# Optimization experiments

Hardware: AMD Instinct MI355X
Metric: run time of the kernel (lower is better)

Reference implementation:

```python
import jax, jax.numpy as jnp
import numpy as np

N = 8          # num_nodes (forced: stack with deconv output of leading dim 64 = 8*8)
T = 10         # out_dim == num_steps (Conv1d(out_dim, 1, ...) runs over the time axis)
H = 64         # hidden_dim (forced: ConvTranspose1d in_channels=64)
E = 2 * N      # edges come in fwd/rev pairs; E/2 must equal N for avg_pool squeeze
NODE_IN = 512  # gat1 in_dim = x_feat width (510) + CNN_1 output (2)
EDGE_IN = 128


def _conv1d(x, w, b, pad):
    # x: [B, Cin, L], w: [Cout, Cin, K]
    y = jax.lax.conv_general_dilated(x, w, (1,), [(pad, pad)],
                                     dimension_numbers=('NCH', 'OIH', 'NCH'))
    return y + b[None, :, None]


def _gat(x, src, dst, ea, W, a_s, a_d, We, a_e, bias, heads, ch, concat):
    # PyG GATConv with edge_dim and default add_self_loops=True (mean-fill edge_attr)
    n = x.shape[0]
    loop = jnp.arange(n)
    src = jnp.concatenate([src, loop])
    dst = jnp.concatenate([dst, loop])
    ea = jnp.concatenate([ea, jnp.broadcast_to(ea.mean(0), (n, ea.shape[1]))], 0)
    h = (x @ W).reshape(n, heads, ch)                 # [N,H,C]
    he = (ea @ We).reshape(-1, heads, ch)             # [E+N,H,C]
    alpha = (h * a_s).sum(-1)[src] + (h * a_d).sum(-1)[dst] + (he * a_e).sum(-1)
    alpha = jax.nn.leaky_relu(alpha, 0.2)             # [E+N,H]
    amax = jax.ops.segment_max(alpha, dst, num_segments=n)
    ex = jnp.exp(alpha - amax[dst])
    den = jax.ops.segment_sum(ex, dst, num_segments=n)
    w = ex / (den[dst] + 1e-16)                       # scatter-softmax over dst
    out = jax.ops.segment_sum(w[:, :, None] * h[src], dst, num_segments=n)
    out = out.reshape(n, heads * ch) if concat else out.mean(1)
    return out + bias


def _forward(x_feat, x_feat_tmp, edge_attr, c1w1, c1b1, c1w2, c1b2,
             g1_lin, g1_as, g1_ad, g1_le, g1_ae, g1_b,
             g2_lin, g2_as, g2_ad, g2_le, g2_ae, g2_b,
             mlp_w1, mlp_b1, mlp_w2, mlp_b2,
             d1w, d1b, d2w, d2b, d3w, d3b,
             c2w1, c2b1, c2w2, c2b2, c2l1w, c2l1b, c2l2w, c2l2b,
             edge_index):
    src, dst = edge_index[0], edge_index[1]
    # ---- CNN_1 on rows 1 and 5 of x_feat_tmp ----
    t = jnp.stack([x_feat_tmp[1], x_feat_tmp[5]], axis=1)    # [N,2,T]
    t = t.reshape(2, N, T)                                   # torch .view semantics
    t = jax.nn.relu(_conv1d(t, c1w1, c1b1, 1))               # [2,N,T]
    t = _conv1d(jnp.transpose(t, (0, 2, 1)), c1w2, c1b2, 1)  # [2,1,N]
    x_ = jax.nn.relu(t.reshape(N, 2))                        # torch .view semantics
    # ---- GAT stack ----
    x = jnp.concatenate([x_feat, x_], axis=1)                # [N,512]
    x = jax.nn.relu(_gat(x, src, dst, edge_attr, g1_lin, g1_as, g1_ad,
                         g1_le, g1_ae, g1_b, 4, H, True))    # [N,256]
    ea_new = jax.nn.relu(edge_attr @ mlp_w1 + mlp_b1) @ mlp_w2 + mlp_b2  # [E,64]
    x = jax.nn.relu(_gat(x, src, dst, ea_new, g2_lin, g2_as, g2_ad,
                         g2_le, g2_ae, g2_b, 1, H, False))   # [N,64]
    # ---- ConvTranspose1d on length-1 input == einsum; avg_pool2d over nodes/edges ----
    x_pool = (jnp.einsum('ni,iot->not', x, d1w) + d1b[None, :, None]).mean(0)          # [64,10]
    ef = (jnp.einsum('ni,iot->not', ea_new[::2], d2w) + d2b[None, :, None]).mean(0)    # [64,10]
    er = (jnp.einsum('ni,iot->not', ea_new[1::2], d3w) + d3b[None, :, None]).mean(0)   # [64,10]
    inf = x_feat_tmp.reshape(N * N, T)                       # [64,10]
    # ---- CNN_2 ----
    c = jnp.stack([x_pool, inf, ef, er], axis=1)             # [64,4,10]
    c = _conv1d(c, c2w1, c2b1, 0)                            # [64,32,8]
    c = c.reshape(N * N, 32, 4, 2).max(-1)                   # MaxPool1d(2) -> [64,32,4]
    c = _conv1d(c, c2w2, c2b2, 0)                            # [64,64,2]
    c = c.reshape(N * N, 128)                                # Flatten(1,2)
    c = jax.nn.relu((c @ c2l1w + c2l1b) @ c2l2w + c2l2b)     # [64,10]
    return c.reshape(N, N, T)


def setup_inputs():
    ks = iter(jax.random.split(jax.random.key(0), 48))
    def rn(shape, s=0.1):
        return jax.random.normal(next(ks), shape, dtype=jnp.float32) * s
    return dict(
        x_feat=rn((N, NODE_IN - 2), 1.0),
        x_feat_tmp=rn((N, N, T), 1.0),
        edge_attr=rn((E, EDGE_IN), 1.0),
        c1w1=rn((N, N, 3)), c1b1=rn((N,)),
        c1w2=rn((1, T, 3)), c1b2=rn((1,)),
        g1_lin=rn((NODE_IN, 4 * H)), g1_as=rn((4, H)), g1_ad=rn((4, H)),
        g1_le=rn((EDGE_IN, 4 * H)), g1_ae=rn((4, H)), g1_b=rn((4 * H,)),
        g2_lin=rn((4 * H, H)), g2_as=rn((1, H)), g2_ad=rn((1, H)),
        g2_le=rn((H, H)), g2_ae=rn((1, H)), g2_b=rn((H,)),
        mlp_w1=rn((EDGE_IN, H)), mlp_b1=rn((H,)),
        mlp_w2=rn((H, H)), mlp_b2=rn((H,)),
        d1w=rn((H, H, 10)), d1b=rn((H,)),
        d2w=rn((H, H, 10)), d2b=rn((H,)),
        d3w=rn((H, H, 10)), d3b=rn((H,)),
        c2w1=rn((32, 4, 3)), c2b1=rn((32,)),
        c2w2=rn((64, 32, 3)), c2b2=rn((64,)),
        c2l1w=rn((128, 256)), c2l1b=rn((256,)),
        c2l2w=rn((256, T)), c2l2b=rn((T,)),
        edge_index=jax.random.randint(next(ks), (2, E), 0, N, dtype=jnp.int32),
    )


def reference(x_feat, x_feat_tmp, edge_attr, c1w1, c1b1, c1w2, c1b2,
              g1_lin, g1_as, g1_ad, g1_le, g1_ae, g1_b,
              g2_lin, g2_as, g2_ad, g2_le, g2_ae, g2_b,
              mlp_w1, mlp_b1, mlp_w2, mlp_b2,
              d1w, d1b, d2w, d2b, d3w, d3b,
              c2w1, c2b1, c2w2, c2b2, c2l1w, c2l1b, c2l2w, c2l2b,
              edge_index):
    return _forward(x_feat, x_feat_tmp, edge_attr, c1w1, c1b1, c1w2, c1b2,
                    g1_lin, g1_as, g1_ad, g1_le, g1_ae, g1_b,
                    g2_lin, g2_as, g2_ad, g2_le, g2_ae, g2_b,
                    mlp_w1, mlp_b1, mlp_w2, mlp_b2,
                    d1w, d1b, d2w, d2b, d3w, d3b,
                    c2w1, c2b1, c2w2, c2b2, c2l1w, c2l1b, c2l2w, c2l2b,
                    edge_index)
```

## Files before the change

### kernel.cpp

```cpp
#include <hip/hip_runtime.h>
#include <math.h>

#define WS_HXPART 0
#define WS_SMALL  8192
#define SM_XCNN 0
#define SM_SE1A 16
#define SM_SE1B 84
#define SM_SE2  152
#define SM_WF   172
#define SM_BF   1452
#define SM_VME  1462
#define SM_SIZE 1600

#define F_H    0
#define F_X1   2048
#define F_H2P  4096
#define F_GL0  6144
#define F_GL1  6400
#define F_G1AS 6656
#define F_G1AD 6912
#define F_G1B  7168
#define F_SS1  7424
#define F_SD1  7456
#define F_MX1  7488
#define F_DN1  7520
#define F_WT1  7552
#define F_SW2  7680
#define F_A1   7680
#define F_H2   7936
#define F_X2   8448
#define F_G2AS 8960
#define F_G2AD 9024
#define F_G2B  9088
#define F_SS2  9152
#define F_SD2  9160
#define F_MX2  9168
#define F_DN2  9176
#define F_A2   9184
#define F_WT2  9248
#define F_SML  13824
#define F_SW1  15424
#define F_CIN  15808
#define F_ESRC 15968
#define F_EDST 15992
#define F_SB1  16016
#define F_SB2  16048
#define F_SDB  16112
#define F_VM0  16128
#define SM_TOT 16192

__global__ __launch_bounds__(256) void k1_pre(
    const float* __restrict__ xf,   const float* __restrict__ xft,
    const float* __restrict__ ea,
    const float* __restrict__ c1w1, const float* __restrict__ c1b1,
    const float* __restrict__ c1w2, const float* __restrict__ c1b2,
    const float* __restrict__ g1lin,const float* __restrict__ g1le,
    const float* __restrict__ g1ae,
    const float* __restrict__ mw1,  const float* __restrict__ mb1,
    const float* __restrict__ mw2,  const float* __restrict__ mb2,
    const float* __restrict__ g2le, const float* __restrict__ g2ae,
    const float* __restrict__ l1w,  const float* __restrict__ l1b,
    const float* __restrict__ l2w,  const float* __restrict__ l2b,
    float* __restrict__ ws)
{
    const int b = blockIdx.x, tid = threadIdx.x;
    if (b < 4) {
        __shared__ float sx[1024];
        const int k0 = b * 128;
        const int klen = (b == 3) ? 126 : 128;
        for (int idx = tid; idx < 1024; idx += 256) {
            int n = idx >> 7, kk = idx & 127;
            sx[n * 128 + kk] = (kk < klen) ? xf[n * 510 + k0 + kk] : 0.f;
        }
        __syncthreads();
        float acc[8];
        #pragma unroll
        for (int n = 0; n < 8; ++n) acc[n] = 0.f;
        for (int kk = 0; kk < 128; ++kk) {
            float w = g1lin[(k0 + kk) * 256 + tid];
            #pragma unroll
            for (int n = 0; n < 8; ++n) acc[n] += sx[n * 128 + kk] * w;
        }
        #pragma unroll
        for (int n = 0; n < 8; ++n)
            ws[WS_HXPART + ((n * 256 + tid) << 2) + b] = acc[n];
    } else if (b < 6) {
        __shared__ float seaC[1088];
        __shared__ float sae[256], q1h[256];
        const int kh = b - 4, k0 = kh * 64;
        for (int idx = tid; idx < 1024; idx += 256) {
            int e = idx >> 6, kk = idx & 63;
            seaC[e * 64 + kk] = ea[e * 128 + k0 + kk];
        }
        sae[tid] = g1ae[tid];
        __syncthreads();
        if (tid < 64) {
            float m = 0.f;
            for (int e = 0; e < 16; ++e) m += seaC[e * 64 + tid];
            seaC[1024 + tid] = m * (1.f / 16.f);
        }
        __syncthreads();
        {
            int kk = tid >> 2, hd = tid & 3;
            float acc = 0.f;
            for (int c = 0; c < 64; ++c)
                acc += g1le[(k0 + kk) * 256 + hd * 64 + c] * sae[hd * 64 + c];
            q1h[tid] = acc;
        }
        __syncthreads();
        if (tid < 68) {
            int e = tid >> 2, hd = tid & 3;
            int row = (tid < 64) ? e : 16;
            if (tid >= 64) hd = tid - 64;
            float acc = 0.f;
            for (int kk = 0; kk < 64; ++kk) acc += seaC[row * 64 + kk] * q1h[kk * 4 + hd];
            int dst = (tid < 64) ? tid : (64 + hd);
            ws[WS_SMALL + ((kh == 0) ? SM_SE1A : SM_SE1B) + dst] = acc;
        }
    } else if (b == 6) {
        __shared__ float sea[2048];
        __shared__ float tmp[1024];
        __shared__ float ean[17 * 64];
        __shared__ float sq2a[64], sq2[64];
        for (int idx = tid; idx < 2048; idx += 256) sea[idx] = ea[idx];
        if (tid < 64) sq2a[tid] = g2ae[tid];
        __syncthreads();
        for (int o = tid; o < 1024; o += 256) {
            int e = o >> 6, c = o & 63;
            float acc = mb1[c];
            for (int k = 0; k < 128; ++k) acc += sea[e * 128 + k] * mw1[k * 64 + c];
            tmp[o] = fmaxf(acc, 0.f);
        }
        __syncthreads();
        for (int o = tid; o < 1024; o += 256) {
            int e = o >> 6, c = o & 63;
            float acc = mb2[c];
            for (int k = 0; k < 64; ++k) acc += tmp[e * 64 + k] * mw2[k * 64 + c];
            ean[o] = acc;
        }
        __syncthreads();
        if (tid < 64) {
            float m = 0.f;
            for (int e = 0; e < 16; ++e) m += ean[e * 64 + tid];
            ean[1024 + tid] = m * (1.f / 16.f);
        } else if (tid < 128) {
            int c = tid - 64;
            float m = 0.f;
            for (int e = 0; e < 16; e += 2) m += ean[e * 64 + c];
            ws[WS_SMALL + SM_VME + c] = m * 0.125f;
        } else if (tid < 192) {
            int c = tid - 128;
            float m = 0.f;
            for (int e = 1; e < 16; e += 2) m += ean[e * 64 + c];
            ws[WS_SMALL + SM_VME + 64 + c] = m * 0.125f;
        }
        __syncthreads();
        if (tid < 64) {
            float acc = 0.f;
            for (int c = 0; c < 64; ++c) acc += g2le[tid * 64 + c] * sq2a[c];
            sq2[tid] = acc;
        }
        __syncthreads();
        if (tid < 16) {
            float acc = 0.f;
            for (int k = 0; k < 64; ++k) acc += ean[tid * 64 + k] * sq2[k];
            ws[WS_SMALL + SM_SE2 + tid] = acc;
        } else if (tid == 16) {
            float acc = 0.f;
            for (int k = 0; k < 64; ++k) acc += ean[1024 + k] * sq2[k];
            ws[WS_SMALL + SM_SE2 + 16] = acc;
        }
    } else if (b == 7) {
        __shared__ float t2[160], y1[160], y2[16];
        if (tid < 160) {
            int b_ = tid / 80, ch = (tid % 80) / 10, tt = tid % 10;
            int srow = ((ch & 1) == 0) ? 1 : 5;
            int n = 4 * b_ + (ch >> 1);
            t2[tid] = xft[srow * 80 + n * 10 + tt];
        }
        __syncthreads();
        if (tid < 160) {
            int b_ = tid / 80, co = (tid % 80) / 10, tt = tid % 10;
            float acc = c1b1[co];
            for (int ci = 0; ci < 8; ++ci)
                for (int k = 0; k < 3; ++k) {
                    int p = tt + k - 1;
                    if (p >= 0 && p < 10) acc += t2[b_ * 80 + ci * 10 + p] * c1w1[co * 24 + ci * 3 + k];
                }
            y1[tid] = fmaxf(acc, 0.f);
        }
        __syncthreads();
        if (tid < 16) {
            int b_ = tid >> 3, p = tid & 7;
            float acc = c1b2[0];
            for (int i = 0; i < 10; ++i)
                for (int k = 0; k < 3; ++k) {
                    int q = p + k - 1;
                    if (q >= 0 && q < 8) acc += y1[b_ * 80 + q * 10 + i] * c1w2[i * 3 + k];
                }
            y2[tid] = acc;
        }
        __syncthreads();
        if (tid < 16) ws[WS_SMALL + SM_XCNN + tid] = fmaxf(y2[tid], 0.f);
    } else {
        __shared__ float sl2[2560];
        for (int idx = tid; idx < 2560; idx += 256) sl2[idx] = l2w[idx];
        __syncthreads();
        const int m0 = (b - 8) * 32;
        for (int o = tid; o < 320; o += 256) {
            int ml = o / 10, t = o % 10, m = m0 + ml;
            float acc = 0.f;
            for (int j = 0; j < 256; ++j) acc += l1w[m * 256 + j] * sl2[j * 10 + t];
            ws[WS_SMALL + SM_WF + m * 10 + t] = acc;
        }
        if (b == 8 && tid < 10) {
            float acc = l2b[tid];
            for (int j = 0; j < 256; ++j) acc += l1b[j] * sl2[j * 10 + tid];
            ws[WS_SMALL + SM_BF + tid] = acc;
        }
    }
}

__global__ __launch_bounds__(512) void k2_main(
    const float* __restrict__ xft,
    const float* __restrict__ g1lin,
    const float* __restrict__ g1as, const float* __restrict__ g1ad,
    const float* __restrict__ g1b,
    const float* __restrict__ g2lin,
    const float* __restrict__ g2as, const float* __restrict__ g2ad,
    const float* __restrict__ g2b,
    const int* __restrict__ eidx,
    const float* __restrict__ d1w, const float* __restrict__ d1b,
    const float* __restrict__ d2w, const float* __restrict__ d2b,
    const float* __restrict__ d3w, const float* __restrict__ d3b,
    const float* __restrict__ c2w1, const float* __restrict__ c2b1,
    const float* __restrict__ c2w2, const float* __restrict__ c2b2,
    const float* __restrict__ ws, float* __restrict__ out)
{
    __shared__ float sm[SM_TOT];
    const int tid = threadIdx.x;
    const int r0 = blockIdx.x * 4;
    int* esrc = (int*)sm + F_ESRC;
    int* edst = (int*)sm + F_EDST;

    const int jj = tid & 255, hf = tid >> 8;
    float4 rH[4];
    #pragma unroll
    for (int nl = 0; nl < 4; ++nl)
        rH[nl] = *(const float4*)&ws[WS_HXPART + (((hf * 4 + nl) * 256 + jj) << 2)];
    if (tid < 400)
        *(float4*)&sm[F_SML + tid * 4] = *(const float4*)&ws[WS_SMALL + tid * 4];
    if (tid < 256) {
        sm[F_G1AS + tid] = g1as[tid];
        sm[F_G1AD + tid] = g1ad[tid];
        sm[F_G1B  + tid] = g1b[tid];
        sm[F_GL0  + tid] = g1lin[510 * 256 + tid];
        sm[F_GL1  + tid] = g1lin[511 * 256 + tid];
    } else {
        int j = tid - 256;
        if (j < 64)       { sm[F_G2AS + j] = g2as[j]; sm[F_G2AD + j] = g2ad[j]; sm[F_G2B + j] = g2b[j]; }
        else if (j < 88)  { int i = j - 64;  esrc[i] = (i < 16) ? eidx[i] : i - 16;
                                             edst[i] = (i < 16) ? eidx[16 + i] : i - 16; }
        else if (j < 128) { int i = j - 88;  int rl = i / 10, t = i % 10;
                            sm[F_CIN + rl * 40 + 10 + t] = xft[(r0 + rl) * 10 + t]; }
        else if (j < 160) sm[F_SB1 + j - 128] = c2b1[j - 128];
        else if (j < 224) sm[F_SB2 + j - 160] = c2b2[j - 160];
        else if (j < 236) { int i = j - 224, tau = i / 4, rl = i % 4;
                            const float* db = (tau == 0) ? d1b : (tau == 1) ? d2b : d3b;
                            sm[F_SDB + i] = db[r0 + rl]; }
    }
    for (int idx = tid; idx < 384; idx += 512) sm[F_SW1 + idx] = c2w1[idx];
    float rA[15], rW[12];
    {
        int ii = tid / 40, rem = tid - (tid / 40) * 40;
        #pragma unroll
        for (int i = 0; i < 15; ++i) {
            const float* dw = (ii < 64) ? d1w : (ii < 128) ? d2w : d3w;
            rA[i] = dw[(ii & 63) * 640 + r0 * 10 + rem];
            ii += 12; rem += 32; if (rem >= 40) { rem -= 40; ++ii; }
        }
    }
    #pragma unroll
    for (int i = 0; i < 12; ++i) rW[i] = c2w2[tid + 512 * i];
    {
        float p0 = g2lin[tid * 32], p1 = g2lin[tid * 32 + 16];
        asm volatile("" :: "v"(p0), "v"(p1));
    }
    __syncthreads();

    #pragma unroll
    for (int nl = 0; nl < 4; ++nl) {
        int n = hf * 4 + nl;
        float acc = ((rH[nl].x + rH[nl].y) + rH[nl].z) + rH[nl].w;
        acc += sm[F_SML + SM_XCNN + n * 2] * sm[F_GL0 + jj]
             + sm[F_SML + SM_XCNN + n * 2 + 1] * sm[F_GL1 + jj];
        sm[F_H + n * 256 + jj] = acc;
    }
    __syncthreads();
    {
        int p = tid >> 4, g = tid & 15, n = p >> 2, hd = p & 3;
        float aS = 0.f, aD = 0.f;
        #pragma unroll
        for (int cc = 0; cc < 4; ++cc) {
            int c = (((cc + p) & 3) << 4) + g;
            float hv = sm[F_H + n * 256 + hd * 64 + c];
            aS += hv * sm[F_G1AS + hd * 64 + c];
            aD += hv * sm[F_G1AD + hd * 64 + c];
        }
        #pragma unroll
        for (int m = 8; m >= 1; m >>= 1) { aS += __shfl_xor(aS, m); aD += __shfl_xor(aD, m); }
        if (g == 0) { sm[F_SS1 + p] = aS; sm[F_SD1 + p] = aD; }
    }
    __syncthreads();
    {
        int p = tid >> 4, g = tid & 15, n = p >> 2, hd = p & 3;
        #define AL1(e) ({ int _e = (e); \
            float _se = (_e < 16) ? (sm[F_SML+SM_SE1A+_e*4+hd] + sm[F_SML+SM_SE1B+_e*4+hd]) \
                                  : (sm[F_SML+SM_SE1A+64+hd]   + sm[F_SML+SM_SE1B+64+hd]); \
            float _s = sm[F_SS1 + esrc[_e]*4+hd] + sm[F_SD1 + edst[_e]*4+hd] + _se; \
            (_s > 0.f) ? _s : 0.2f * _s; })
        float v1 = (edst[g] == n) ? AL1(g) : -1e30f;
        float v2 = (g < 8 && edst[g + 16] == n) ? AL1(g + 16) : -1e30f;
        float mx = fmaxf(v1, v2);
        #pragma unroll
        for (int m = 8; m >= 1; m >>= 1) mx = fmaxf(mx, __shfl_xor(mx, m));
        float ex = expf(v1 - mx) + ((g < 8) ? expf(v2 - mx) : 0.f);
        #pragma unroll
        for (int m = 8; m >= 1; m >>= 1) ex += __shfl_xor(ex, m);
        if (g == 0) { sm[F_MX1 + p] = mx; sm[F_DN1 + p] = ex; }
    }
    __syncthreads();
    if (tid < 96) {
        int e = tid >> 2, hd = tid & 3, d = edst[e];
        float al = AL1(e);
        sm[F_WT1 + tid] = expf(al - sm[F_MX1 + d * 4 + hd]) / (sm[F_DN1 + d * 4 + hd] + 1e-16f);
        #undef AL1
    }
    __syncthreads();
    if (tid < 256) {
        int s = tid >> 5, n = (tid >> 2) & 7, hd = tid & 3;
        float acc = 0.f;
        #pragma unroll
        for (int e = 0; e < 24; ++e)
            acc += (edst[e] == n && esrc[e] == s) ? sm[F_WT1 + e * 4 + hd] : 0.f;
        sm[F_A1 + tid] = acc;
    }
    __syncthreads();
    {
        const int hd = jj >> 6;
        #pragma unroll
        for (int nl = 0; nl < 4; ++nl) {
            int n = hf * 4 + nl;
            float acc = 0.f;
            #pragma unroll
            for (int s = 0; s < 8; ++s)
                acc += sm[F_A1 + s * 32 + n * 4 + hd] * sm[F_H + s * 256 + jj];
            sm[F_X1 + n * 256 + jj] = fmaxf(acc + sm[F_G1B + jj], 0.f);
        }
    }
    __syncthreads();
    {
        const int kc = tid >> 7, sub = (tid >> 6) & 1, c = tid & 63;
        float p0 = 0.f, p1 = 0.f, p2 = 0.f, p3 = 0.f;
        for (int kk = 0; kk < 64; ++kk) {
            int k = kc * 64 + kk;
            float g = g2lin[k * 64 + c];
            p0 += sm[F_X1 + (sub * 4 + 0) * 256 + k] * g;
            p1 += sm[F_X1 + (sub * 4 + 1) * 256 + k] * g;
            p2 += sm[F_X1 + (sub * 4 + 2) * 256 + k] * g;
            p3 += sm[F_X1 + (sub * 4 + 3) * 256 + k] * g;
        }
        sm[F_H2P + kc * 512 + (sub * 4 + 0) * 64 + c] = p0;
        sm[F_H2P + kc * 512 + (sub * 4 + 1) * 64 + c] = p1;
        sm[F_H2P + kc * 512 + (sub * 4 + 2) * 64 + c] = p2;
        sm[F_H2P + kc * 512 + (sub * 4 + 3) * 64 + c] = p3;
        #pragma unroll
        for (int i = 4; i < 12; ++i) sm[F_SW2 + tid + 512 * i] = rW[i];
    }
    __syncthreads();
    {
        int n = tid >> 6, c = tid & 63;
        float hv = sm[F_H2P + n * 64 + c] + sm[F_H2P + 512 + n * 64 + c]
                 + sm[F_H2P + 1024 + n * 64 + c] + sm[F_H2P + 1536 + n * 64 + c];
        sm[F_H2 + n * 64 + c] = hv;
        float aS = hv * sm[F_G2AS + c], aD = hv * sm[F_G2AD + c];
        #pragma unroll
        for (int m = 32; m >= 1; m >>= 1) { aS += __shfl_xor(aS, m); aD += __shfl_xor(aD, m); }
        if (c == 0) { sm[F_SS2 + n] = aS; sm[F_SD2 + n] = aD; }
    }
    __syncthreads();
    {
        #define AL2(e) ({ int _e = (e); \
            float _s = sm[F_SS2 + esrc[_e]] + sm[F_SD2 + edst[_e]] \
                     + sm[F_SML + SM_SE2 + ((_e < 16) ? _e : 16)]; \
            (_s > 0.f) ? _s : 0.2f * _s; })
        if (tid < 256) {
            int n = tid >> 5, g = tid & 31;
            float v = (g < 24 && edst[g] == n) ? AL2(g) : -1e30f;
            float mx = v;
            #pragma unroll
            for (int m = 16; m >= 1; m >>= 1) mx = fmaxf(mx, __shfl_xor(mx, m));
            float ex = expf(v - mx);
            #pragma unroll
            for (int m = 16; m >= 1; m >>= 1) ex += __shfl_xor(ex, m);
            if (g == 0) { sm[F_MX2 + n] = mx; sm[F_DN2 + n] = ex; }
        }
    }
    __syncthreads();
    if (tid < 24) {
        int d = edst[tid];
        float al = AL2(tid);
        sm[F_WT2 + tid] = expf(al - sm[F_MX2 + d]) / (sm[F_DN2 + d] + 1e-16f);
        #undef AL2
    }
    __syncthreads();
    if (tid < 64) {
        int n = tid >> 3, s = tid & 7;
        float acc = 0.f;
        #pragma unroll
        for (int e = 0; e < 24; ++e)
            acc += (edst[e] == n && esrc[e] == s) ? sm[F_WT2 + e] : 0.f;
        sm[F_A2 + tid] = acc;
    }
    __syncthreads();
    {
        int n = tid >> 6, c = tid & 63;
        float acc = 0.f;
        #pragma unroll
        for (int s = 0; s < 8; ++s) acc += sm[F_A2 + n * 8 + s] * sm[F_H2 + s * 64 + c];
        sm[F_X2 + n * 64 + c] = fmaxf(acc + sm[F_G2B + c], 0.f);
    }
    __syncthreads();
    if (tid < 64) {
        float m = 0.f;
        #pragma unroll
        for (int n = 0; n < 8; ++n) m += sm[F_X2 + n * 64 + tid];
        sm[F_VM0 + tid] = m * 0.125f;
    }
    __syncthreads();

    #pragma unroll
    for (int i = 0; i < 15; ++i) sm[tid + 512 * i] = rA[i];
    #pragma unroll
    for (int i = 0; i < 4; ++i) sm[F_SW2 + tid + 512 * i] = rW[i];
    __syncthreads();
    if (tid < 480) {
        int o = tid >> 2, q = tid & 3;
        int t = o % 10, tau = (o / 10) % 3, rl = o / 30;
        float acc = 0.f;
        for (int i = q * 16; i < q * 16 + 16; ++i) {
            float vm = (tau == 0) ? sm[F_VM0 + i]
                     : (tau == 1) ? sm[F_SML + SM_VME + i]
                                  : sm[F_SML + SM_VME + 64 + i];
            acc += vm * sm[(tau * 64 + i) * 40 + rl * 10 + t];
        }
        acc += __shfl_xor(acc, 2); acc += __shfl_xor(acc, 1);
        if (q == 0) {
            int ch = (tau == 0) ? 0 : (tau + 1);
            sm[F_CIN + rl * 40 + ch * 10 + t] = acc + sm[F_SDB + tau * 4 + rl];
        }
    }
    __syncthreads();
    for (int o = tid; o < 1024; o += 512) {
        int rl = o >> 8, co = (o >> 3) & 31, p = o & 7;
        float acc = sm[F_SB1 + co];
        #pragma unroll
        for (int ci = 0; ci < 4; ++ci)
            #pragma unroll
            for (int k = 0; k < 3; ++k)
                acc += sm[F_CIN + rl * 40 + ci * 10 + p + k] * sm[F_SW1 + co * 12 + ci * 3 + k];
        sm[4096 + o] = acc;
    }
    __syncthreads();
    {
        int rl = tid >> 7, m = tid & 127, co2 = m >> 1, p = m & 1;
        float acc = sm[F_SB2 + co2];
        for (int ci = 0; ci < 32; ++ci)
            #pragma unroll
            for (int k = 0; k < 3; ++k) {
                int u0 = 4096 + rl * 256 + ci * 8 + 2 * (p + k);
                acc += fmaxf(sm[u0], sm[u0 + 1]) * sm[F_SW2 + co2 * 96 + ci * 3 + k];
            }
        sm[1024 + rl * 128 + m] = acc;
    }
    __syncthreads();
    if (tid < 320) {
        int o = tid >> 3, l = tid & 7;
        int rl = o / 10, t = o % 10;
        float acc = 0.f;
        for (int m = l * 16; m < l * 16 + 16; ++m)
            acc += sm[1024 + rl * 128 + m] * sm[F_SML + SM_WF + m * 10 + t];
        acc += __shfl_xor(acc, 4); acc += __shfl_xor(acc, 2); acc += __shfl_xor(acc, 1);
        if (l == 0)
            out[(r0 + rl) * 10 + t] = fmaxf(acc + sm[F_SML + SM_BF + t], 0.f);
    }
}

extern "C" void kernel_launch(void* const* d_in, const int* in_sizes, int n_in,
                              void* d_out, int out_size, void* d_ws, size_t ws_size,
                              hipStream_t stream)
{
    const float* xf    = (const float*)d_in[0];
    const float* xft   = (const float*)d_in[1];
    const float* ea    = (const float*)d_in[2];
    const float* c1w1  = (const float*)d_in[3];
    const float* c1b1  = (const float*)d_in[4];
    const float* c1w2  = (const float*)d_in[5];
    const float* c1b2  = (const float*)d_in[6];
    const float* g1lin = (const float*)d_in[7];
    const float* g1as  = (const float*)d_in[8];
    const float* g1ad  = (const float*)d_in[9];
    const float* g1le  = (const float*)d_in[10];
    const float* g1ae  = (const float*)d_in[11];
    const float* g1b   = (const float*)d_in[12];
    const float* g2lin = (const float*)d_in[13];
    const float* g2as  = (const float*)d_in[14];
    const float* g2ad  = (const float*)d_in[15];
    const float* g2le  = (const float*)d_in[16];
    const float* g2ae  = (const float*)d_in[17];
    const float* g2b   = (const float*)d_in[18];
    const float* mw1   = (const float*)d_in[19];
    const float* mb1   = (const float*)d_in[20];
    const float* mw2   = (const float*)d_in[21];
    const float* mb2   = (const float*)d_in[22];
    const float* d1w   = (const float*)d_in[23];
    const float* d1b   = (const float*)d_in[24];
    const float* d2w   = (const float*)d_in[25];
    const float* d2b   = (const float*)d_in[26];
    const float* d3w   = (const float*)d_in[27];
    const float* d3b   = (const float*)d_in[28];
    const float* c2w1  = (const float*)d_in[29];
    const float* c2b1  = (const float*)d_in[30];
    const float* c2w2  = (const float*)d_in[31];
    const float* c2b2  = (const float*)d_in[32];
    const float* l1w   = (const float*)d_in[33];
    const float* l1b   = (const float*)d_in[34];
    const float* l2w   = (const float*)d_in[35];
    const float* l2b   = (const float*)d_in[36];
    const int*   eidx  = (const int*)d_in[37];
    float* ws  = (float*)d_ws;
    float* out = (float*)d_out;

    hipLaunchKernelGGL(k1_pre, dim3(12), dim3(256), 0, stream,
        xf, xft, ea, c1w1, c1b1, c1w2, c1b2,
        g1lin, g1le, g1ae, mw1, mb1, mw2, mb2,
        g2le, g2ae, l1w, l1b, l2w, l2b, ws);
    hipLaunchKernelGGL(k2_main, dim3(16), dim3(512), 0, stream,
        xft, g1lin, g1as, g1ad, g1b,
        g2lin, g2as, g2ad, g2b, eidx,
        d1w, d1b, d2w, d2b, d3w, d3b,
        c2w1, c2b1, c2w2, c2b2, ws, out);
}
```

Baseline: 33.46 us.

## Fuse pre and main kernels with a global atomic-flag grid barrier

Merges the preprocessing kernel and the main kernel into one 16-block launch. A device-scope atomic counter in the workspace acts as a grid barrier between the phases. The x@W1 product is now split into 16 K-chunks of 32, one per block, and the main phase reduces 16 partial sums instead of 4. This removes one kernel launch gap and lets the weight register prefetch overlap the pre-phase, at the cost of an extra memset and a spin-wait that relies on all 16 blocks being resident at the same time.

```diff
diff --git a/kernel.cpp b/kernel.cpp
--- a/kernel.cpp
+++ b/kernel.cpp
@@ -2,7 +2,7 @@
 #include <math.h>
 
 #define WS_HXPART 0
-#define WS_SMALL  8192
+#define WS_SMALL  32768
 #define SM_XCNN 0
 #define SM_SE1A 16
 #define SM_SE1B 84
@@ -10,7 +10,7 @@
 #define SM_WF   172
 #define SM_BF   1452
 #define SM_VME  1462
-#define SM_SIZE 1600
+#define WS_FLAGS 34368
 
 #define F_H    0
 #define F_X1   2048
@@ -48,209 +48,58 @@
 #define F_SDB  16112
 #define F_VM0  16128
 #define SM_TOT 16192
-
-__global__ __launch_bounds__(256) void k1_pre(
+#define F_SX   4608
+
+__global__ __launch_bounds__(512) void fused_all(
     const float* __restrict__ xf,   const float* __restrict__ xft,
     const float* __restrict__ ea,
     const float* __restrict__ c1w1, const float* __restrict__ c1b1,
     const float* __restrict__ c1w2, const float* __restrict__ c1b2,
     const float* __restrict__ g1lin,const float* __restrict__ g1le,
     const float* __restrict__ g1ae,
-    const float* __restrict__ mw1,  const float* __restrict__ mb1,
-    const float* __restrict__ mw2,  const float* __restrict__ mb2,
-    const float* __restrict__ g2le, const float* __restrict__ g2ae,
-    const float* __restrict__ l1w,  const float* __restrict__ l1b,
-    const float* __restrict__ l2w,  const float* __restrict__ l2b,
-    float* __restrict__ ws)
-{
-    const int b = blockIdx.x, tid = threadIdx.x;
-    if (b < 4) {
-        __shared__ float sx[1024];
-        const int k0 = b * 128;
-        const int klen = (b == 3) ? 126 : 128;
-        for (int idx = tid; idx < 1024; idx += 256) {
-            int n = idx >> 7, kk = idx & 127;
-            sx[n * 128 + kk] = (kk < klen) ? xf[n * 510 + k0 + kk] : 0.f;
-        }
-        __syncthreads();
-        float acc[8];
-        #pragma unroll
-        for (int n = 0; n < 8; ++n) acc[n] = 0.f;
-        for (int kk = 0; kk < 128; ++kk) {
-            float w = g1lin[(k0 + kk) * 256 + tid];
-            #pragma unroll
-            for (int n = 0; n < 8; ++n) acc[n] += sx[n * 128 + kk] * w;
-        }
-        #pragma unroll
-        for (int n = 0; n < 8; ++n)
-            ws[WS_HXPART + ((n * 256 + tid) << 2) + b] = acc[n];
-    } else if (b < 6) {
-        __shared__ float seaC[1088];
-        __shared__ float sae[256], q1h[256];
-        const int kh = b - 4, k0 = kh * 64;
-        for (int idx = tid; idx < 1024; idx += 256) {
-            int e = idx >> 6, kk = idx & 63;
-            seaC[e * 64 + kk] = ea[e * 128 + k0 + kk];
-        }
-        sae[tid] = g1ae[tid];
-        __syncthreads();
-        if (tid < 64) {
-            float m = 0.f;
-            for (int e = 0; e < 16; ++e) m += seaC[e * 64 + tid];
-            seaC[1024 + tid] = m * (1.f / 16.f);
-        }
-        __syncthreads();
-        {
-            int kk = tid >> 2, hd = tid & 3;
-            float acc = 0.f;
-            for (int c = 0; c < 64; ++c)
-                acc += g1le[(k0 + kk) * 256 + hd * 64 + c] * sae[hd * 64 + c];
-            q1h[tid] = acc;
-        }
-        __syncthreads();
-        if (tid < 68) {
-            int e = tid >> 2, hd = tid & 3;
-            int row = (tid < 64) ? e : 16;
-            if (tid >= 64) hd = tid - 64;
-            float acc = 0.f;
-            for (int kk = 0; kk < 64; ++kk) acc += seaC[row * 64 + kk] * q1h[kk * 4 + hd];
-            int dst = (tid < 64) ? tid : (64 + hd);
-            ws[WS_SMALL + ((kh == 0) ? SM_SE1A : SM_SE1B) + dst] = acc;
-        }
-    } else if (b == 6) {
-        __shared__ float sea[2048];
-        __shared__ float tmp[1024];
-        __shared__ float ean[17 * 64];
-        __shared__ float sq2a[64], sq2[64];
-        for (int idx = tid; idx < 2048; idx += 256) sea[idx] = ea[idx];
-        if (tid < 64) sq2a[tid] = g2ae[tid];
-        __syncthreads();
-        for (int o = tid; o < 1024; o += 256) {
-            int e = o >> 6, c = o & 63;
-            float acc = mb1[c];
-            for (int k = 0; k < 128; ++k) acc += sea[e * 128 + k] * mw1[k * 64 + c];
-            tmp[o] = fmaxf(acc, 0.f);
-        }
-        __syncthreads();
-        for (int o = tid; o < 1024; o += 256) {
-            int e = o >> 6, c = o & 63;
-            float acc = mb2[c];
-            for (int k = 0; k < 64; ++k) acc += tmp[e * 64 + k] * mw2[k * 64 + c];
-            ean[o] = acc;
-        }
-        __syncthreads();
-        if (tid < 64) {
-            float m = 0.f;
-            for (int e = 0; e < 16; ++e) m += ean[e * 64 + tid];
-            ean[1024 + tid] = m * (1.f / 16.f);
-        } else if (tid < 128) {
-            int c = tid - 64;
-            float m = 0.f;
-            for (int e = 0; e < 16; e += 2) m += ean[e * 64 + c];
-            ws[WS_SMALL + SM_VME + c] = m * 0.125f;
-        } else if (tid < 192) {
-            int c = tid - 128;
-            float m = 0.f;
-            for (int e = 1; e < 16; e += 2) m += ean[e * 64 + c];
-            ws[WS_SMALL + SM_VME + 64 + c] = m * 0.125f;
-        }
-        __syncthreads();
-        if (tid < 64) {
-            float acc = 0.f;
-            for (int c = 0; c < 64; ++c) acc += g2le[tid * 64 + c] * sq2a[c];
-            sq2[tid] = acc;
-        }
-        __syncthreads();
-        if (tid < 16) {
-            float acc = 0.f;
-            for (int k = 0; k < 64; ++k) acc += ean[tid * 64 + k] * sq2[k];
-            ws[WS_SMALL + SM_SE2 + tid] = acc;
-        } else if (tid == 16) {
-            float acc = 0.f;
-            for (int k = 0; k < 64; ++k) acc += ean[1024 + k] * sq2[k];
-            ws[WS_SMALL + SM_SE2 + 16] = acc;
-        }
-    } else if (b == 7) {
-        __shared__ float t2[160], y1[160], y2[16];
-        if (tid < 160) {
-            int b_ = tid / 80, ch = (tid % 80) / 10, tt = tid % 10;
-            int srow = ((ch & 1) == 0) ? 1 : 5;
-            int n = 4 * b_ + (ch >> 1);
-            t2[tid] = xft[srow * 80 + n * 10 + tt];
-        }
-        __syncthreads();
-        if (tid < 160) {
-            int b_ = tid / 80, co = (tid % 80) / 10, tt = tid % 10;
-            float acc = c1b1[co];
-            for (int ci = 0; ci < 8; ++ci)
-                for (int k = 0; k < 3; ++k) {
-                    int p = tt + k - 1;
-                    if (p >= 0 && p < 10) acc += t2[b_ * 80 + ci * 10 + p] * c1w1[co * 24 + ci * 3 + k];
-                }
-            y1[tid] = fmaxf(acc, 0.f);
-        }
-        __syncthreads();
-        if (tid < 16) {
-            int b_ = tid >> 3, p = tid & 7;
-            float acc = c1b2[0];
-            for (int i = 0; i < 10; ++i)
-                for (int k = 0; k < 3; ++k) {
-                    int q = p + k - 1;
-                    if (q >= 0 && q < 8) acc += y1[b_ * 80 + q * 10 + i] * c1w2[i * 3 + k];
-                }
-            y2[tid] = acc;
-        }
-        __syncthreads();
-        if (tid < 16) ws[WS_SMALL + SM_XCNN + tid] = fmaxf(y2[tid], 0.f);
-    } else {
-        __shared__ float sl2[2560];
-        for (int idx = tid; idx < 2560; idx += 256) sl2[idx] = l2w[idx];
-        __syncthreads();
-        const int m0 = (b - 8) * 32;
-        for (int o = tid; o < 320; o += 256) {
-            int ml = o / 10, t = o % 10, m = m0 + ml;
-            float acc = 0.f;
-            for (int j = 0; j < 256; ++j) acc += l1w[m * 256 + j] * sl2[j * 10 + t];
-            ws[WS_SMALL + SM_WF + m * 10 + t] = acc;
-        }
-        if (b == 8 && tid < 10) {
-            float acc = l2b[tid];
-            for (int j = 0; j < 256; ++j) acc += l1b[j] * sl2[j * 10 + tid];
-            ws[WS_SMALL + SM_BF + tid] = acc;
-        }
-    }
-}
-
-__global__ __launch_bounds__(512) void k2_main(
-    const float* __restrict__ xft,
-    const float* __restrict__ g1lin,
     const float* __restrict__ g1as, const float* __restrict__ g1ad,
     const float* __restrict__ g1b,
     const float* __restrict__ g2lin,
     const float* __restrict__ g2as, const float* __restrict__ g2ad,
+    const float* __restrict__ g2le, const float* __restrict__ g2ae,
     const float* __restrict__ g2b,
-    const int* __restrict__ eidx,
-    const float* __restrict__ d1w, const float* __restrict__ d1b,
-    const float* __restrict__ d2w, const float* __restrict__ d2b,
-    const float* __restrict__ d3w, const float* __restrict__ d3b,
+    const float* __restrict__ mw1,  const float* __restrict__ mb1,
+    const float* __restrict__ mw2,  const float* __restrict__ mb2,
+    const float* __restrict__ d1w,  const float* __restrict__ d1b,
+    const float* __restrict__ d2w,  const float* __restrict__ d2b,
+    const float* __restrict__ d3w,  const float* __restrict__ d3b,
     const float* __restrict__ c2w1, const float* __restrict__ c2b1,
     const float* __restrict__ c2w2, const float* __restrict__ c2b2,
-    const float* __restrict__ ws, float* __restrict__ out)
+    const float* __restrict__ l1w,  const float* __restrict__ l1b,
+    const float* __restrict__ l2w,  const float* __restrict__ l2b,
+    const int* __restrict__ eidx,
+    float* __restrict__ ws, float* __restrict__ out)
 {
     __shared__ float sm[SM_TOT];
-    const int tid = threadIdx.x;
-    const int r0 = blockIdx.x * 4;
+    const int tid = threadIdx.x, b = blockIdx.x;
+    const int r0 = b * 4;
+    const int jj = tid & 255, hf = tid >> 8;
     int* esrc = (int*)sm + F_ESRC;
     int* edst = (int*)sm + F_EDST;
-
-    const int jj = tid & 255, hf = tid >> 8;
-    float4 rH[4];
+    int* flag = (int*)(ws + WS_FLAGS);
+
+    float rA[15], rW[12];
+    {
+        int ii = tid / 40, rem = tid - (tid / 40) * 40;
+        #pragma unroll
+        for (int i = 0; i < 15; ++i) {
+            const float* dw = (ii < 64) ? d1w : (ii < 128) ? d2w : d3w;
+            rA[i] = dw[(ii & 63) * 640 + r0 * 10 + rem];
+            ii += 12; rem += 32; if (rem >= 40) { rem -= 40; ++ii; }
+        }
+    }
     #pragma unroll
-    for (int nl = 0; nl < 4; ++nl)
-        rH[nl] = *(const float4*)&ws[WS_HXPART + (((hf * 4 + nl) * 256 + jj) << 2)];
-    if (tid < 400)
-        *(float4*)&sm[F_SML + tid * 4] = *(const float4*)&ws[WS_SMALL + tid * 4];
+    for (int i = 0; i < 12; ++i) rW[i] = c2w2[tid + 512 * i];
+    const int k0 = b * 32;
+    const int klen = (b == 15) ? 30 : 32;
     if (tid < 256) {
+        int n = tid >> 5, kk = tid & 31;
+        sm[F_SX + tid] = (kk < klen) ? xf[n * 510 + k0 + kk] : 0.f;
         sm[F_G1AS + tid] = g1as[tid];
         sm[F_G1AD + tid] = g1ad[tid];
         sm[F_G1B  + tid] = g1b[tid];
@@ -270,28 +119,187 @@
                             sm[F_SDB + i] = db[r0 + rl]; }
     }
     for (int idx = tid; idx < 384; idx += 512) sm[F_SW1 + idx] = c2w1[idx];
-    float rA[15], rW[12];
-    {
-        int ii = tid / 40, rem = tid - (tid / 40) * 40;
-        #pragma unroll
-        for (int i = 0; i < 15; ++i) {
-            const float* dw = (ii < 64) ? d1w : (ii < 128) ? d2w : d3w;
-            rA[i] = dw[(ii & 63) * 640 + r0 * 10 + rem];
-            ii += 12; rem += 32; if (rem >= 40) { rem -= 40; ++ii; }
-        }
-    }
-    #pragma unroll
-    for (int i = 0; i < 12; ++i) rW[i] = c2w2[tid + 512 * i];
     {
         float p0 = g2lin[tid * 32], p1 = g2lin[tid * 32 + 16];
         asm volatile("" :: "v"(p0), "v"(p1));
     }
+    __syncthreads();
+
+    {
+        float w[32];
+        #pragma unroll
+        for (int kk = 0; kk < 32; ++kk) w[kk] = g1lin[(k0 + kk) * 256 + jj];
+        #pragma unroll
+        for (int nl = 0; nl < 4; ++nl) {
+            int n = hf * 4 + nl;
+            float acc = 0.f;
+            #pragma unroll
+            for (int kk = 0; kk < 32; ++kk) acc += sm[F_SX + n * 32 + kk] * w[kk];
+            ws[WS_HXPART + (n * 256 + jj) * 16 + b] = acc;
+        }
+    }
+
+    if (b < 2) {
+        float* seaC = sm;
+        float* sae  = sm + 1088;
+        float* q1h  = sm + 1344;
+        const int kh = b, kq0 = kh * 64;
+        for (int idx = tid; idx < 1024; idx += 512) {
+            int e = idx >> 6, kk = idx & 63;
+            seaC[e * 64 + kk] = ea[e * 128 + kq0 + kk];
+        }
+        if (tid < 256) sae[tid] = g1ae[tid];
+        __syncthreads();
+        if (tid < 64) {
+            float m = 0.f;
+            for (int e = 0; e < 16; ++e) m += seaC[e * 64 + tid];
+            seaC[1024 + tid] = m * (1.f / 16.f);
+        }
+        __syncthreads();
+        if (tid < 256) {
+            int kk = tid >> 2, hd = tid & 3;
+            float acc = 0.f;
+            for (int c = 0; c < 64; ++c)
+                acc += g1le[(kq0 + kk) * 256 + hd * 64 + c] * sae[hd * 64 + c];
+            q1h[tid] = acc;
+        }
+        __syncthreads();
+        if (tid < 68) {
+            int e = tid >> 2, hd = tid & 3;
+            int row = (tid < 64) ? e : 16;
+            if (tid >= 64) hd = tid - 64;
+            float acc = 0.f;
+            for (int kk = 0; kk < 64; ++kk) acc += seaC[row * 64 + kk] * q1h[kk * 4 + hd];
+            int dst = (tid < 64) ? tid : (64 + hd);
+            ws[WS_SMALL + ((kh == 0) ? SM_SE1A : SM_SE1B) + dst] = acc;
+        }
+    } else if (b == 2) {
+        float* sea = sm;
+        float* tmp = sm + 2048;
+        float* ean = sm + 3072;
+        float* sq2a = sm + 4160;
+        float* sq2  = sm + 4224;
+        for (int idx = tid; idx < 2048; idx += 512) sea[idx] = ea[idx];
+        if (tid < 64) sq2a[tid] = g2ae[tid];
+        __syncthreads();
+        for (int o = tid; o < 1024; o += 512) {
+            int e = o >> 6, c = o & 63;
+            float acc = mb1[c];
+            for (int k = 0; k < 128; ++k) acc += sea[e * 128 + k] * mw1[k * 64 + c];
+            tmp[o] = fmaxf(acc, 0.f);
+        }
+        __syncthreads();
+        for (int o = tid; o < 1024; o += 512) {
+            int e = o >> 6, c = o & 63;
+            float acc = mb2[c];
+            for (int k = 0; k < 64; ++k) acc += tmp[e * 64 + k] * mw2[k * 64 + c];
+            ean[o] = acc;
+        }
+        __syncthreads();
+        if (tid < 64) {
+            float m = 0.f;
+            for (int e = 0; e < 16; ++e) m += ean[e * 64 + tid];
+            ean[1024 + tid] = m * (1.f / 16.f);
+        } else if (tid < 128) {
+            int c = tid - 64;
+            float m = 0.f;
+            for (int e = 0; e < 16; e += 2) m += ean[e * 64 + c];
+            ws[WS_SMALL + SM_VME + c] = m * 0.125f;
+        } else if (tid < 192) {
+            int c = tid - 128;
+            float m = 0.f;
+            for (int e = 1; e < 16; e += 2) m += ean[e * 64 + c];
+            ws[WS_SMALL + SM_VME + 64 + c] = m * 0.125f;
+        } else if (tid < 256) {
+            int c = tid - 192;
+            float acc = 0.f;
+            for (int cc = 0; cc < 64; ++cc) acc += g2le[c * 64 + cc] * sq2a[cc];
+            sq2[c] = acc;
+        }
+        __syncthreads();
+        if (tid < 16) {
+            float acc = 0.f;
+            for (int k = 0; k < 64; ++k) acc += ean[tid * 64 + k] * sq2[k];
+            ws[WS_SMALL + SM_SE2 + tid] = acc;
+        } else if (tid == 16) {
+            float acc = 0.f;
+            for (int k = 0; k < 64; ++k) acc += ean[1024 + k] * sq2[k];
+            ws[WS_SMALL + SM_SE2 + 16] = acc;
+        }
+    } else if (b == 3) {
+        float* t2 = sm;
+        float* y1 = sm + 160;
+        if (tid < 160) {
+            int b_ = tid / 80, ch = (tid % 80) / 10, tt = tid % 10;
+            int srow = ((ch & 1) == 0) ? 1 : 5;
+            int n = 4 * b_ + (ch >> 1);
+            t2[tid] = xft[srow * 80 + n * 10 + tt];
+        }
+        __syncthreads();
+        if (tid < 160) {
+            int b_ = tid / 80, co = (tid % 80) / 10, tt = tid % 10;
+            float acc = c1b1[co];
+            for (int ci = 0; ci < 8; ++ci)
+                for (int k = 0; k < 3; ++k) {
+                    int p = tt + k - 1;
+                    if (p >= 0 && p < 10) acc += t2[b_ * 80 + ci * 10 + p] * c1w1[co * 24 + ci * 3 + k];
+                }
+            y1[tid] = fmaxf(acc, 0.f);
+        }
+        __syncthreads();
+        if (tid < 16) {
+            int b_ = tid >> 3, p = tid & 7;
+            float acc = c1b2[0];
+            for (int i = 0; i < 10; ++i)
+                for (int k = 0; k < 3; ++k) {
+                    int q = p + k - 1;
+                    if (q >= 0 && q < 8) acc += y1[b_ * 80 + q * 10 + i] * c1w2[i * 3 + k];
+                }
+            ws[WS_SMALL + SM_XCNN + tid] = fmaxf(acc, 0.f);
+        }
+    } else if (b < 12) {
+        float* sl2 = sm;
+        for (int idx = tid; idx < 2560; idx += 512) sl2[idx] = l2w[idx];
+        __syncthreads();
+        const int m0 = (b - 4) * 16;
+        if (tid < 160) {
+            int ml = tid / 10, t = tid % 10, m = m0 + ml;
+            float acc = 0.f;
+            for (int j = 0; j < 256; ++j) acc += l1w[m * 256 + j] * sl2[j * 10 + t];
+            ws[WS_SMALL + SM_WF + m * 10 + t] = acc;
+        } else if (b == 4 && tid < 170) {
+            int t = tid - 160;
+            float acc = l2b[t];
+            for (int j = 0; j < 256; ++j) acc += l1b[j] * sl2[j * 10 + t];
+            ws[WS_SMALL + SM_BF + t] = acc;
+        }
+    }
+
+    __syncthreads();
+    __threadfence();
+    if (tid == 0) __hip_atomic_fetch_add(flag, 1, __ATOMIC_RELEASE, __HIP_MEMORY_SCOPE_AGENT);
+    if (tid == 0)
+        while (__hip_atomic_load(flag, __ATOMIC_ACQUIRE, __HIP_MEMORY_SCOPE_AGENT) < 16)
+            __builtin_amdgcn_s_sleep(1);
+    __syncthreads();
+    __threadfence();
+
+    float4 rH[4][4];
+    #pragma unroll
+    for (int nl = 0; nl < 4; ++nl)
+        #pragma unroll
+        for (int q = 0; q < 4; ++q)
+            rH[nl][q] = *(const float4*)&ws[WS_HXPART + ((hf * 4 + nl) * 256 + jj) * 16 + q * 4];
+    if (tid < 400)
+        *(float4*)&sm[F_SML + tid * 4] = *(const float4*)&ws[WS_SMALL + tid * 4];
     __syncthreads();
 
     #pragma unroll
     for (int nl = 0; nl < 4; ++nl) {
         int n = hf * 4 + nl;
-        float acc = ((rH[nl].x + rH[nl].y) + rH[nl].z) + rH[nl].w;
+        float4 a = rH[nl][0], b4 = rH[nl][1], c4 = rH[nl][2], d4 = rH[nl][3];
+        float acc = ((a.x + a.y) + (a.z + a.w)) + ((b4.x + b4.y) + (b4.z + b4.w))
+                  + ((c4.x + c4.y) + (c4.z + c4.w)) + ((d4.x + d4.y) + (d4.z + d4.w));
         acc += sm[F_SML + SM_XCNN + n * 2] * sm[F_GL0 + jj]
              + sm[F_SML + SM_XCNN + n * 2 + 1] * sm[F_GL1 + jj];
         sm[F_H + n * 256 + jj] = acc;
@@ -541,13 +549,14 @@
     float* ws  = (float*)d_ws;
     float* out = (float*)d_out;
 
-    hipLaunchKernelGGL(k1_pre, dim3(12), dim3(256), 0, stream,
+    hipMemsetAsync((char*)d_ws + WS_FLAGS * sizeof(float), 0, 8, stream);
+
+    hipLaunchKernelGGL(fused_all, dim3(16), dim3(512), 0, stream,
         xf, xft, ea, c1w1, c1b1, c1w2, c1b2,
-        g1lin, g1le, g1ae, mw1, mb1, mw2, mb2,
-        g2le, g2ae, l1w, l1b, l2w, l2b, ws);
-    hipLaunchKernelGGL(k2_main, dim3(16), dim3(512), 0, stream,
-        xft, g1lin, g1as, g1ad, g1b,
-        g2lin, g2as, g2ad, g2b, eidx,
+        g1lin, g1le, g1ae, g1as, g1ad, g1b,
+        g2lin, g2as, g2ad, g2le, g2ae, g2b,
+        mw1, mb1, mw2, mb2,
         d1w, d1b, d2w, d2b, d3w, d3b,
-        c2w1, c2b1, c2w2, c2b2, ws, out);
+        c2w1, c2b1, c2w2, c2b2,
+        l1w, l1b, l2w, l2b, eidx, ws, out);
 }
```

Result: slower. 42.06 us (+25.7%).
